# Kernel optimization log

Measured on AMD Instinct MI355X. Metric: run time of the kernel, lower is better.

Reference implementation:

```python
import jax, jax.numpy as jnp
import numpy as np

B, I, O, T, L = 16, 512, 512, 256, 4096
EPS = 1e-8


def setup_inputs() -> dict:
    key = jax.random.key(0)
    ks = jax.random.split(key, 10)
    def lin_w(k, out_d, in_d):  # kaiming-uniform-ish init like torch Linear
        bound = 1.0 / np.sqrt(in_d)
        return jax.random.uniform(k, (out_d, in_d), jnp.float32, -bound, bound)
    return {
        "x": jax.random.normal(ks[0], (B, I, L), jnp.float32),
        "t": jax.random.normal(ks[1], (B, T), jnp.float32),
        "weight": lin_w(ks[2], O, I),            # base conv weight [O, I]
        "W1": lin_w(ks[3], T, T), "b1": jnp.zeros((T,), jnp.float32),
        "W2": lin_w(ks[4], T, T), "b2": jnp.zeros((T,), jnp.float32),
        "W3": lin_w(ks[5], I, T), "b3": jnp.zeros((I,), jnp.float32),
    }


def reference(x, t, weight, W1, b1, W2, b2, W3, b3):
    # mod MLP: Linear -> SiLU -> Linear -> SiLU -> Linear
    h = jax.nn.silu(t @ W1.T + b1)
    h = jax.nn.silu(h @ W2.T + b2)
    s = h @ W3.T + b3 + 1.0                    # [B, I] modulation scales
    bw = weight[None, :, :] * s[:, None, :]    # [B, O, I]
    demod = jax.lax.rsqrt(jnp.sum(bw * bw, axis=2) + EPS)  # [B, O]
    bw = bw * demod[:, :, None]                # demodulated per-sample weights
    # grouped 1x1 conv (groups=B) == batched pointwise contraction
    return jnp.einsum('boi,bil->bol', bw, x)   # [B, O, L]
```

## Files before the change

kernel.cpp:

```cpp
#include <hip/hip_runtime.h>
#include <hip/hip_bf16.h>

typedef float f4v __attribute__((ext_vector_type(4)));
typedef float f32x4 __attribute__((ext_vector_type(4)));
typedef __bf16 bf16x8 __attribute__((ext_vector_type(8)));

#define GLDS16(gsrc, ldst)                                                  \
  __builtin_amdgcn_global_load_lds(                                         \
      (const __attribute__((address_space(1))) unsigned int*)(gsrc),        \
      (__attribute__((address_space(3))) unsigned int*)(ldst), 16, 0, 0)

__device__ __forceinline__ unsigned pack2bf(float lo, float hi) {
  unsigned short ua = __builtin_bit_cast(unsigned short, (__bf16)lo);
  unsigned short ub = __builtin_bit_cast(unsigned short, (__bf16)hi);
  return (unsigned)ua | ((unsigned)ub << 16);
}

__global__ __launch_bounds__(256) void mlp_kernel(
    const float* __restrict__ t,
    const float* __restrict__ W1, const float* __restrict__ b1,
    const float* __restrict__ W2, const float* __restrict__ b2,
    const float* __restrict__ W3, const float* __restrict__ b3,
    float* __restrict__ s_out) {
  __shared__ float tt[256];
  __shared__ float hh[256];
  const int b = blockIdx.x;
  const int tid = threadIdx.x;
  tt[tid] = t[b * 256 + tid];
  __syncthreads();
  float acc = b1[tid];
  {
    const f4v* wrow = (const f4v*)(W1 + tid * 256);
    #pragma unroll 16
    for (int k = 0; k < 64; ++k) {
      f4v wv = wrow[k];
      acc += wv[0] * tt[4 * k] + wv[1] * tt[4 * k + 1] +
             wv[2] * tt[4 * k + 2] + wv[3] * tt[4 * k + 3];
    }
  }
  float h = acc / (1.0f + expf(-acc));
  __syncthreads();
  hh[tid] = h;
  __syncthreads();
  acc = b2[tid];
  {
    const f4v* wrow = (const f4v*)(W2 + tid * 256);
    #pragma unroll 16
    for (int k = 0; k < 64; ++k) {
      f4v wv = wrow[k];
      acc += wv[0] * hh[4 * k] + wv[1] * hh[4 * k + 1] +
             wv[2] * hh[4 * k + 2] + wv[3] * hh[4 * k + 3];
    }
  }
  h = acc / (1.0f + expf(-acc));
  __syncthreads();
  tt[tid] = h;
  __syncthreads();
  #pragma unroll
  for (int rep = 0; rep < 2; ++rep) {
    const int o = rep * 256 + tid;
    float a3 = b3[o];
    const f4v* wrow = (const f4v*)(W3 + o * 256);
    #pragma unroll 16
    for (int k = 0; k < 64; ++k) {
      f4v wv = wrow[k];
      a3 += wv[0] * tt[4 * k] + wv[1] * tt[4 * k + 1] +
            wv[2] * tt[4 * k + 2] + wv[3] * tt[4 * k + 3];
    }
    s_out[b * 512 + o] = a3 + 1.0f;
  }
}

__global__ __launch_bounds__(256) void modw_kernel(
    const float* __restrict__ weight, const float* __restrict__ s_in,
    unsigned short* __restrict__ bwq) {
  const int tid = threadIdx.x;
  const int wid = (blockIdx.x << 2) | (tid >> 6);
  const int b = wid >> 9;
  const int o = wid & 511;
  const int lane = tid & 63;
  const f4v* wp = (const f4v*)(weight + o * 512 + lane * 8);
  const f4v* sp = (const f4v*)(s_in + b * 512 + lane * 8);
  f4v w0 = wp[0], w1 = wp[1];
  f4v s0 = sp[0], s1 = sp[1];
  float p[8];
  p[0] = w0[0] * s0[0]; p[1] = w0[1] * s0[1];
  p[2] = w0[2] * s0[2]; p[3] = w0[3] * s0[3];
  p[4] = w1[0] * s1[0]; p[5] = w1[1] * s1[1];
  p[6] = w1[2] * s1[2]; p[7] = w1[3] * s1[3];
  float ss = 0.0f;
  #pragma unroll
  for (int i = 0; i < 8; ++i) ss += p[i] * p[i];
  #pragma unroll
  for (int off = 32; off; off >>= 1) ss += __shfl_xor(ss, off);
  const float d = rsqrtf(ss + 1e-8f);
  uint4 outw;
  outw.x = pack2bf(p[0] * d, p[1] * d);
  outw.y = pack2bf(p[2] * d, p[3] * d);
  outw.z = pack2bf(p[4] * d, p[5] * d);
  outw.w = pack2bf(p[6] * d, p[7] * d);
  *(uint4*)(bwq + ((size_t)(b * 512 + o)) * 512 + lane * 8) = outw;
}

__global__ __launch_bounds__(256, 2) void gemm_kernel(
    const float* __restrict__ x, const unsigned short* __restrict__ bwq,
    float* __restrict__ out) {
  __shared__ __align__(16) unsigned short As[2][128 * 32];
  __shared__ __align__(16) unsigned short Bs[128 * 32];

  const int bid = blockIdx.x;
  const int swz = ((bid & 7) << 8) | (bid >> 3);
  const int mt = swz & 3;
  const int nt = (swz >> 2) & 31;
  const int bb = swz >> 7;

  const int tid = threadIdx.x;
  const int lane = tid & 63;
  const int wv = tid >> 6;
  const int wr = wv >> 1, wc = wv & 1;

  const unsigned short* abase = bwq + ((size_t)(bb * 512 + mt * 128)) * 512;
  const float* xbase = x + ((size_t)bb * 512) * 4096 + nt * 128;

  const int pq = tid >> 5;
  const int lc = tid & 31;
  const float* xp = xbase + (size_t)(pq * 4) * 4096 + lc * 4;
  const int sw_w = (lc & 3) << 4;
  char* BsB = (char*)Bs;

  const int g0 = tid, g1 = 256 + tid;
  const unsigned short* asrc0 = abase + (g0 >> 2) * 512 + (g0 & 3) * 8;
  const unsigned short* asrc1 = abase + (g1 >> 2) * 512 + (g1 & 3) * 8;

  const int arow = wr * 64 + (lane & 15);
  const int kgo = (lane >> 4) * 8;
  const int nrow0 = wc * 64 + (lane & 15);
  const int sb = (nrow0 >> 2) & 3;
  const int bByte = nrow0 * 64 + (((lane >> 4) ^ sb) << 4);

  f32x4 acc[4][4] = {};

  GLDS16(asrc0, &As[0][g0 * 8]);
  GLDS16(asrc1, &As[0][g1 * 8]);
  f4v v0 = *(const f4v*)(xp);
  f4v v1 = *(const f4v*)(xp + 4096);
  f4v v2 = *(const f4v*)(xp + 8192);
  f4v v3 = *(const f4v*)(xp + 12288);
  f4v t0, t1, t2, t3;

  for (int it = 0; it < 16; ++it) {
    const int cur = it & 1;
    {
      float r0[4] = {v0[0], v0[1], v0[2], v0[3]};
      float r1[4] = {v1[0], v1[1], v1[2], v1[3]};
      float r2[4] = {v2[0], v2[1], v2[2], v2[3]};
      float r3[4] = {v3[0], v3[1], v3[2], v3[3]};
      #pragma unroll
      for (int j = 0; j < 4; ++j) {
        uint2 val;
        val.x = pack2bf(r0[j], r1[j]);
        val.y = pack2bf(r2[j], r3[j]);
        const int n = (lc << 2) + j;
        *(uint2*)(BsB + n * 64 + ((pq * 8) ^ sw_w)) = val;
      }
    }
    __syncthreads();

    if (it < 15) {
      const int k0n = (it + 1) << 5;
      const unsigned short* an0 = asrc0 + k0n;
      const unsigned short* an1 = asrc1 + k0n;
      GLDS16(an0, &As[cur ^ 1][g0 * 8]);
      GLDS16(an1, &As[cur ^ 1][g1 * 8]);
      const float* xn = xp + (size_t)k0n * 4096;
      t0 = *(const f4v*)(xn);
      t1 = *(const f4v*)(xn + 4096);
      t2 = *(const f4v*)(xn + 8192);
      t3 = *(const f4v*)(xn + 12288);
    }

    {
      const unsigned short* ab = &As[cur][0];
      bf16x8 a0 = *(const bf16x8*)(ab + arow * 32 + kgo);
      bf16x8 a1 = *(const bf16x8*)(ab + arow * 32 + 512 + kgo);
      bf16x8 a2 = *(const bf16x8*)(ab + arow * 32 + 1024 + kgo);
      bf16x8 a3 = *(const bf16x8*)(ab + arow * 32 + 1536 + kgo);
      bf16x8 bf0 = *(const bf16x8*)(BsB + bByte);
      bf16x8 bf1 = *(const bf16x8*)(BsB + bByte + 1024);
      bf16x8 bf2 = *(const bf16x8*)(BsB + bByte + 2048);
      bf16x8 bf3 = *(const bf16x8*)(BsB + bByte + 3072);
      acc[0][0] = __builtin_amdgcn_mfma_f32_16x16x32_bf16(a0, bf0, acc[0][0], 0, 0, 0);
      acc[0][1] = __builtin_amdgcn_mfma_f32_16x16x32_bf16(a0, bf1, acc[0][1], 0, 0, 0);
      acc[0][2] = __builtin_amdgcn_mfma_f32_16x16x32_bf16(a0, bf2, acc[0][2], 0, 0, 0);
      acc[0][3] = __builtin_amdgcn_mfma_f32_16x16x32_bf16(a0, bf3, acc[0][3], 0, 0, 0);
      acc[1][0] = __builtin_amdgcn_mfma_f32_16x16x32_bf16(a1, bf0, acc[1][0], 0, 0, 0);
      acc[1][1] = __builtin_amdgcn_mfma_f32_16x16x32_bf16(a1, bf1, acc[1][1], 0, 0, 0);
      acc[1][2] = __builtin_amdgcn_mfma_f32_16x16x32_bf16(a1, bf2, acc[1][2], 0, 0, 0);
      acc[1][3] = __builtin_amdgcn_mfma_f32_16x16x32_bf16(a1, bf3, acc[1][3], 0, 0, 0);
      acc[2][0] = __builtin_amdgcn_mfma_f32_16x16x32_bf16(a2, bf0, acc[2][0], 0, 0, 0);
      acc[2][1] = __builtin_amdgcn_mfma_f32_16x16x32_bf16(a2, bf1, acc[2][1], 0, 0, 0);
      acc[2][2] = __builtin_amdgcn_mfma_f32_16x16x32_bf16(a2, bf2, acc[2][2], 0, 0, 0);
      acc[2][3] = __builtin_amdgcn_mfma_f32_16x16x32_bf16(a2, bf3, acc[2][3], 0, 0, 0);
      acc[3][0] = __builtin_amdgcn_mfma_f32_16x16x32_bf16(a3, bf0, acc[3][0], 0, 0, 0);
      acc[3][1] = __builtin_amdgcn_mfma_f32_16x16x32_bf16(a3, bf1, acc[3][1], 0, 0, 0);
      acc[3][2] = __builtin_amdgcn_mfma_f32_16x16x32_bf16(a3, bf2, acc[3][2], 0, 0, 0);
      acc[3][3] = __builtin_amdgcn_mfma_f32_16x16x32_bf16(a3, bf3, acc[3][3], 0, 0, 0);
    }
    __syncthreads();

    if (it < 15) { v0 = t0; v1 = t1; v2 = t2; v3 = t3; }
  }

  const size_t ob =
      ((size_t)(bb * 512 + mt * 128 + wr * 64 + ((lane >> 4) << 2))) * 4096 +
      nt * 128 + wc * 64 + (lane & 15);
  #pragma unroll
  for (int mi = 0; mi < 4; ++mi)
    #pragma unroll
    for (int ni = 0; ni < 4; ++ni)
      #pragma unroll
      for (int jj = 0; jj < 4; ++jj)
        out[ob + (size_t)(mi * 16 + jj) * 4096 + ni * 16] = acc[mi][ni][jj];
}

extern "C" void kernel_launch(void* const* d_in, const int* in_sizes, int n_in,
                              void* d_out, int out_size, void* d_ws, size_t ws_size,
                              hipStream_t stream) {
  const float* x      = (const float*)d_in[0];
  const float* t      = (const float*)d_in[1];
  const float* weight = (const float*)d_in[2];
  const float* W1     = (const float*)d_in[3];
  const float* b1     = (const float*)d_in[4];
  const float* W2     = (const float*)d_in[5];
  const float* b2     = (const float*)d_in[6];
  const float* W3     = (const float*)d_in[7];
  const float* b3     = (const float*)d_in[8];
  float* out = (float*)d_out;

  float* s_ws = (float*)d_ws;
  unsigned short* bwq = (unsigned short*)((char*)d_ws + 32 * 1024);

  mlp_kernel<<<16, 256, 0, stream>>>(t, W1, b1, W2, b2, W3, b3, s_ws);
  modw_kernel<<<2048, 256, 0, stream>>>(weight, s_ws, bwq);
  gemm_kernel<<<2048, 256, 0, stream>>>(x, bwq, out);
}
```

Measured before the change: 126.2 us.

## Deepen GEMM pipeline to triple-buffered A, double-buffered B with one barrier

Restructures the batched GEMM main loop into a deeper software pipeline. A tiles are triple-buffered via async global-to-LDS loads, B (x converted to bf16) is double-buffered, and x register prefetch runs three steps ahead. The loop is fully unrolled with hand-placed vmcnt waits so each iteration needs one barrier instead of two. This aims to hide global load latency and cut synchronization stalls. It also raises the launch-bounds occupancy hint to 3, at the cost of more registers and LDS per block and fragile manual waitcnt accounting.

```diff
diff --git a/kernel.cpp b/kernel.cpp
--- a/kernel.cpp
+++ b/kernel.cpp
@@ -102,11 +102,11 @@
   *(uint4*)(bwq + ((size_t)(b * 512 + o)) * 512 + lane * 8) = outw;
 }
 
-__global__ __launch_bounds__(256, 2) void gemm_kernel(
+__global__ __launch_bounds__(256, 3) void gemm_kernel(
     const float* __restrict__ x, const unsigned short* __restrict__ bwq,
     float* __restrict__ out) {
-  __shared__ __align__(16) unsigned short As[2][128 * 32];
-  __shared__ __align__(16) unsigned short Bs[128 * 32];
+  __shared__ __align__(16) unsigned short As[3][128 * 32];
+  __shared__ __align__(16) unsigned short Bs[2][128 * 32];
 
   const int bid = blockIdx.x;
   const int swz = ((bid & 7) << 8) | (bid >> 3);
@@ -139,76 +139,99 @@
   const int bByte = nrow0 * 64 + (((lane >> 4) ^ sb) << 4);
 
   f32x4 acc[4][4] = {};
-
-  GLDS16(asrc0, &As[0][g0 * 8]);
-  GLDS16(asrc1, &As[0][g1 * 8]);
-  f4v v0 = *(const f4v*)(xp);
-  f4v v1 = *(const f4v*)(xp + 4096);
-  f4v v2 = *(const f4v*)(xp + 8192);
-  f4v v3 = *(const f4v*)(xp + 12288);
-  f4v t0, t1, t2, t3;
-
+  f4v xv[3][4];
+
+#define LOADX(SET, STEP)                                                    \
+  do {                                                                      \
+    const float* _p = xp + (size_t)((STEP) * 32) * 4096;                    \
+    xv[SET][0] = *(const f4v*)(_p);                                         \
+    xv[SET][1] = *(const f4v*)(_p + 4096);                                  \
+    xv[SET][2] = *(const f4v*)(_p + 8192);                                  \
+    xv[SET][3] = *(const f4v*)(_p + 12288);                                 \
+  } while (0)
+
+#define STAGEA(STEP, BUF)                                                   \
+  do {                                                                      \
+    GLDS16(asrc0 + (STEP) * 32, &As[BUF][g0 * 8]);                          \
+    GLDS16(asrc1 + (STEP) * 32, &As[BUF][g1 * 8]);                          \
+  } while (0)
+
+#define PACKB(SET, BUF)                                                     \
+  do {                                                                      \
+    char* _bs = BsB + (BUF) * 8192;                                         \
+    _Pragma("unroll")                                                       \
+    for (int j = 0; j < 4; ++j) {                                           \
+      uint2 val;                                                            \
+      val.x = pack2bf(xv[SET][0][j], xv[SET][1][j]);                        \
+      val.y = pack2bf(xv[SET][2][j], xv[SET][3][j]);                        \
+      const int n = (lc << 2) + j;                                          \
+      *(uint2*)(_bs + n * 64 + ((pq * 8) ^ sw_w)) = val;                    \
+    }                                                                       \
+  } while (0)
+
+#define FENCE() asm volatile("" ::: "memory")
+#define BARN(N)                                                             \
+  do {                                                                      \
+    asm volatile("s_waitcnt lgkmcnt(0)\n\ts_waitcnt vmcnt(" #N ")" :::      \
+                     "memory");                                             \
+    __builtin_amdgcn_s_barrier();                                           \
+    asm volatile("" ::: "memory");                                          \
+  } while (0)
+
+#define COMPUTE(CA, CB)                                                     \
+  do {                                                                      \
+    const unsigned short* ab = &As[CA][0];                                  \
+    const char* bbuf = BsB + (CB) * 8192;                                   \
+    bf16x8 a0 = *(const bf16x8*)(ab + arow * 32 + kgo);                     \
+    bf16x8 a1 = *(const bf16x8*)(ab + arow * 32 + 512 + kgo);               \
+    bf16x8 a2 = *(const bf16x8*)(ab + arow * 32 + 1024 + kgo);              \
+    bf16x8 a3 = *(const bf16x8*)(ab + arow * 32 + 1536 + kgo);              \
+    bf16x8 bf0 = *(const bf16x8*)(bbuf + bByte);                            \
+    bf16x8 bf1 = *(const bf16x8*)(bbuf + bByte + 1024);                     \
+    bf16x8 bf2 = *(const bf16x8*)(bbuf + bByte + 2048);                     \
+    bf16x8 bf3 = *(const bf16x8*)(bbuf + bByte + 3072);                     \
+    acc[0][0] = __builtin_amdgcn_mfma_f32_16x16x32_bf16(a0, bf0, acc[0][0], 0, 0, 0); \
+    acc[0][1] = __builtin_amdgcn_mfma_f32_16x16x32_bf16(a0, bf1, acc[0][1], 0, 0, 0); \
+    acc[0][2] = __builtin_amdgcn_mfma_f32_16x16x32_bf16(a0, bf2, acc[0][2], 0, 0, 0); \
+    acc[0][3] = __builtin_amdgcn_mfma_f32_16x16x32_bf16(a0, bf3, acc[0][3], 0, 0, 0); \
+    acc[1][0] = __builtin_amdgcn_mfma_f32_16x16x32_bf16(a1, bf0, acc[1][0], 0, 0, 0); \
+    acc[1][1] = __builtin_amdgcn_mfma_f32_16x16x32_bf16(a1, bf1, acc[1][1], 0, 0, 0); \
+    acc[1][2] = __builtin_amdgcn_mfma_f32_16x16x32_bf16(a1, bf2, acc[1][2], 0, 0, 0); \
+    acc[1][3] = __builtin_amdgcn_mfma_f32_16x16x32_bf16(a1, bf3, acc[1][3], 0, 0, 0); \
+    acc[2][0] = __builtin_amdgcn_mfma_f32_16x16x32_bf16(a2, bf0, acc[2][0], 0, 0, 0); \
+    acc[2][1] = __builtin_amdgcn_mfma_f32_16x16x32_bf16(a2, bf1, acc[2][1], 0, 0, 0); \
+    acc[2][2] = __builtin_amdgcn_mfma_f32_16x16x32_bf16(a2, bf2, acc[2][2], 0, 0, 0); \
+    acc[2][3] = __builtin_amdgcn_mfma_f32_16x16x32_bf16(a2, bf3, acc[2][3], 0, 0, 0); \
+    acc[3][0] = __builtin_amdgcn_mfma_f32_16x16x32_bf16(a3, bf0, acc[3][0], 0, 0, 0); \
+    acc[3][1] = __builtin_amdgcn_mfma_f32_16x16x32_bf16(a3, bf1, acc[3][1], 0, 0, 0); \
+    acc[3][2] = __builtin_amdgcn_mfma_f32_16x16x32_bf16(a3, bf2, acc[3][2], 0, 0, 0); \
+    acc[3][3] = __builtin_amdgcn_mfma_f32_16x16x32_bf16(a3, bf3, acc[3][3], 0, 0, 0); \
+  } while (0)
+
+  STAGEA(0, 0);
+  FENCE();
+  LOADX(0, 0);
+  STAGEA(1, 1);
+  FENCE();
+  LOADX(1, 1);
+  LOADX(2, 2);
+  PACKB(0, 0);
+  BARN(10);
+
+  #pragma unroll
   for (int it = 0; it < 16; ++it) {
-    const int cur = it & 1;
-    {
-      float r0[4] = {v0[0], v0[1], v0[2], v0[3]};
-      float r1[4] = {v1[0], v1[1], v1[2], v1[3]};
-      float r2[4] = {v2[0], v2[1], v2[2], v2[3]};
-      float r3[4] = {v3[0], v3[1], v3[2], v3[3]};
-      #pragma unroll
-      for (int j = 0; j < 4; ++j) {
-        uint2 val;
-        val.x = pack2bf(r0[j], r1[j]);
-        val.y = pack2bf(r2[j], r3[j]);
-        const int n = (lc << 2) + j;
-        *(uint2*)(BsB + n * 64 + ((pq * 8) ^ sw_w)) = val;
-      }
-    }
-    __syncthreads();
-
-    if (it < 15) {
-      const int k0n = (it + 1) << 5;
-      const unsigned short* an0 = asrc0 + k0n;
-      const unsigned short* an1 = asrc1 + k0n;
-      GLDS16(an0, &As[cur ^ 1][g0 * 8]);
-      GLDS16(an1, &As[cur ^ 1][g1 * 8]);
-      const float* xn = xp + (size_t)k0n * 4096;
-      t0 = *(const f4v*)(xn);
-      t1 = *(const f4v*)(xn + 4096);
-      t2 = *(const f4v*)(xn + 8192);
-      t3 = *(const f4v*)(xn + 12288);
-    }
-
-    {
-      const unsigned short* ab = &As[cur][0];
-      bf16x8 a0 = *(const bf16x8*)(ab + arow * 32 + kgo);
-      bf16x8 a1 = *(const bf16x8*)(ab + arow * 32 + 512 + kgo);
-      bf16x8 a2 = *(const bf16x8*)(ab + arow * 32 + 1024 + kgo);
-      bf16x8 a3 = *(const bf16x8*)(ab + arow * 32 + 1536 + kgo);
-      bf16x8 bf0 = *(const bf16x8*)(BsB + bByte);
-      bf16x8 bf1 = *(const bf16x8*)(BsB + bByte + 1024);
-      bf16x8 bf2 = *(const bf16x8*)(BsB + bByte + 2048);
-      bf16x8 bf3 = *(const bf16x8*)(BsB + bByte + 3072);
-      acc[0][0] = __builtin_amdgcn_mfma_f32_16x16x32_bf16(a0, bf0, acc[0][0], 0, 0, 0);
-      acc[0][1] = __builtin_amdgcn_mfma_f32_16x16x32_bf16(a0, bf1, acc[0][1], 0, 0, 0);
-      acc[0][2] = __builtin_amdgcn_mfma_f32_16x16x32_bf16(a0, bf2, acc[0][2], 0, 0, 0);
-      acc[0][3] = __builtin_amdgcn_mfma_f32_16x16x32_bf16(a0, bf3, acc[0][3], 0, 0, 0);
-      acc[1][0] = __builtin_amdgcn_mfma_f32_16x16x32_bf16(a1, bf0, acc[1][0], 0, 0, 0);
-      acc[1][1] = __builtin_amdgcn_mfma_f32_16x16x32_bf16(a1, bf1, acc[1][1], 0, 0, 0);
-      acc[1][2] = __builtin_amdgcn_mfma_f32_16x16x32_bf16(a1, bf2, acc[1][2], 0, 0, 0);
-      acc[1][3] = __builtin_amdgcn_mfma_f32_16x16x32_bf16(a1, bf3, acc[1][3], 0, 0, 0);
-      acc[2][0] = __builtin_amdgcn_mfma_f32_16x16x32_bf16(a2, bf0, acc[2][0], 0, 0, 0);
-      acc[2][1] = __builtin_amdgcn_mfma_f32_16x16x32_bf16(a2, bf1, acc[2][1], 0, 0, 0);
-      acc[2][2] = __builtin_amdgcn_mfma_f32_16x16x32_bf16(a2, bf2, acc[2][2], 0, 0, 0);
-      acc[2][3] = __builtin_amdgcn_mfma_f32_16x16x32_bf16(a2, bf3, acc[2][3], 0, 0, 0);
-      acc[3][0] = __builtin_amdgcn_mfma_f32_16x16x32_bf16(a3, bf0, acc[3][0], 0, 0, 0);
-      acc[3][1] = __builtin_amdgcn_mfma_f32_16x16x32_bf16(a3, bf1, acc[3][1], 0, 0, 0);
-      acc[3][2] = __builtin_amdgcn_mfma_f32_16x16x32_bf16(a3, bf2, acc[3][2], 0, 0, 0);
-      acc[3][3] = __builtin_amdgcn_mfma_f32_16x16x32_bf16(a3, bf3, acc[3][3], 0, 0, 0);
-    }
-    __syncthreads();
-
-    if (it < 15) { v0 = t0; v1 = t1; v2 = t2; v3 = t3; }
+    if (it <= 14) PACKB((it + 1) % 3, (it + 1) & 1);
+    if (it <= 13) STAGEA(it + 2, (it + 2) % 3);
+    FENCE();
+    if (it <= 12) LOADX(it % 3, it + 3);
+    COMPUTE(it % 3, it & 1);
+    if (it <= 12) {
+      BARN(10);
+    } else if (it == 13) {
+      BARN(6);
+    } else if (it == 14) {
+      BARN(0);
+    }
   }
 
   const size_t ob =
@@ -221,6 +244,13 @@
       #pragma unroll
       for (int jj = 0; jj < 4; ++jj)
         out[ob + (size_t)(mi * 16 + jj) * 4096 + ni * 16] = acc[mi][ni][jj];
+
+#undef LOADX
+#undef STAGEA
+#undef PACKB
+#undef FENCE
+#undef BARN
+#undef COMPUTE
 }
 
 extern "C" void kernel_launch(void* const* d_in, const int* in_sizes, int n_in,
```

After: 126.4 us. About the same (+0.2%).

## Pre-transpose and cast x to bf16 in a separate kernel, stream both GEMM operands via LDS DMA

Applied to the files above, without the earlier changes.

Adds a kernel that casts x to bf16 and transposes it to [B, L, I] through an XOR-swizzled LDS tile. The GEMM then loads both A and B tiles with global_load_lds directly into swizzled LDS, with no in-loop register conversion. The GEMM also drops double buffering and the occupancy hint, so loads and MFMA are no longer overlapped within a block. The cost is an extra full pass over x: a 128MB fp32 read plus a 64MB bf16 write and later read.

```diff
diff --git a/kernel.cpp b/kernel.cpp
--- a/kernel.cpp
+++ b/kernel.cpp
@@ -102,11 +102,52 @@
   *(uint4*)(bwq + ((size_t)(b * 512 + o)) * 512 + lane * 8) = outw;
 }
 
-__global__ __launch_bounds__(256, 2) void gemm_kernel(
-    const float* __restrict__ x, const unsigned short* __restrict__ bwq,
-    float* __restrict__ out) {
-  __shared__ __align__(16) unsigned short As[2][128 * 32];
-  __shared__ __align__(16) unsigned short Bs[128 * 32];
+__global__ __launch_bounds__(256) void xcastT_kernel(
+    const float* __restrict__ x, unsigned short* __restrict__ xT) {
+  __shared__ unsigned short lds[64 * 128];
+  const int bidx = blockIdx.x;
+  const int lt = bidx & 63;
+  const int it = (bidx >> 6) & 3;
+  const int b  = bidx >> 8;
+  const int tid = threadIdx.x;
+
+  const int l_lo = tid & 15;
+  const int i_pt = tid >> 4;
+  const float* src =
+      x + ((size_t)(b * 512 + it * 128 + i_pt)) * 4096 + lt * 64 + l_lo * 4;
+  #pragma unroll
+  for (int j = 0; j < 8; ++j) {
+    f4v v = *(const f4v*)(src + (size_t)j * 16 * 4096);
+    const int i = j * 16 + i_pt;
+    const int g = i >> 3;
+    #pragma unroll
+    for (int c = 0; c < 4; ++c) {
+      const int l = l_lo * 4 + c;
+      const int pg = g ^ (l & 15);
+      lds[l * 128 + pg * 8 + (i & 7)] =
+          __builtin_bit_cast(unsigned short, (__bf16)v[c]);
+    }
+  }
+  __syncthreads();
+
+  const int l_loc = tid >> 2;
+  const int iq = tid & 3;
+  unsigned short* dst =
+      xT + ((size_t)(b * 4096 + lt * 64 + l_loc)) * 512 + it * 128;
+  #pragma unroll
+  for (int j = 0; j < 4; ++j) {
+    const int gi = iq * 4 + j;
+    const int pg = gi ^ (l_loc & 15);
+    uint4 val = *(const uint4*)&lds[l_loc * 128 + pg * 8];
+    *(uint4*)(dst + gi * 8) = val;
+  }
+}
+
+__global__ __launch_bounds__(256) void gemm_kernel(
+    const unsigned short* __restrict__ xT,
+    const unsigned short* __restrict__ bwq, float* __restrict__ out) {
+  __shared__ __align__(16) unsigned short As[4096];
+  __shared__ __align__(16) unsigned short Bs[4096];
 
   const int bid = blockIdx.x;
   const int swz = ((bid & 7) << 8) | (bid >> 3);
@@ -120,75 +161,55 @@
   const int wr = wv >> 1, wc = wv & 1;
 
   const unsigned short* abase = bwq + ((size_t)(bb * 512 + mt * 128)) * 512;
-  const float* xbase = x + ((size_t)bb * 512) * 4096 + nt * 128;
-
-  const int pq = tid >> 5;
-  const int lc = tid & 31;
-  const float* xp = xbase + (size_t)(pq * 4) * 4096 + lc * 4;
-  const int sw_w = (lc & 3) << 4;
-  char* BsB = (char*)Bs;
-
-  const int g0 = tid, g1 = 256 + tid;
-  const unsigned short* asrc0 = abase + (g0 >> 2) * 512 + (g0 & 3) * 8;
-  const unsigned short* asrc1 = abase + (g1 >> 2) * 512 + (g1 & 3) * 8;
-
-  const int arow = wr * 64 + (lane & 15);
-  const int kgo = (lane >> 4) * 8;
-  const int nrow0 = wc * 64 + (lane & 15);
-  const int sb = (nrow0 >> 2) & 3;
-  const int bByte = nrow0 * 64 + (((lane >> 4) ^ sb) << 4);
+  const unsigned short* bbase = xT + ((size_t)(bb * 4096 + nt * 128)) * 512;
+
+  const int s0 = tid, s1 = 256 + tid;
+  const int kq0 = s0 >> 7, p0 = s0 & 127;
+  const int kq1 = s1 >> 7, p1 = s1 & 127;
+  const int i0 = p0 ^ ((p0 >> 3) & 7);
+  const int i1 = p1 ^ ((p1 >> 3) & 7);
+  const unsigned short* asrc0 = abase + i0 * 512 + kq0 * 8;
+  const unsigned short* asrc1 = abase + i1 * 512 + kq1 * 8;
+  const unsigned short* bsrc0 = bbase + i0 * 512 + kq0 * 8;
+  const unsigned short* bsrc1 = bbase + i1 * 512 + kq1 * 8;
+  unsigned short* adst0 = As + s0 * 8;
+  unsigned short* adst1 = As + s1 * 8;
+  unsigned short* bdst0 = Bs + s0 * 8;
+  unsigned short* bdst1 = Bs + s1 * 8;
+
+  const int kqL = lane >> 4;
+  const int rL = lane & 15;
+  int aro[4], bro[4];
+  #pragma unroll
+  for (int i = 0; i < 4; ++i) {
+    const int m = wr * 64 + i * 16 + rL;
+    aro[i] = kqL * 2048 + (m ^ ((m >> 3) & 7)) * 16;
+    const int n = wc * 64 + i * 16 + rL;
+    bro[i] = kqL * 2048 + (n ^ ((n >> 3) & 7)) * 16;
+  }
 
   f32x4 acc[4][4] = {};
 
-  GLDS16(asrc0, &As[0][g0 * 8]);
-  GLDS16(asrc1, &As[0][g1 * 8]);
-  f4v v0 = *(const f4v*)(xp);
-  f4v v1 = *(const f4v*)(xp + 4096);
-  f4v v2 = *(const f4v*)(xp + 8192);
-  f4v v3 = *(const f4v*)(xp + 12288);
-  f4v t0, t1, t2, t3;
-
+  #pragma unroll
   for (int it = 0; it < 16; ++it) {
-    const int cur = it & 1;
+    const int ko = it * 32;
+    GLDS16(asrc0 + ko, adst0);
+    GLDS16(asrc1 + ko, adst1);
+    GLDS16(bsrc0 + ko, bdst0);
+    GLDS16(bsrc1 + ko, bdst1);
+    __syncthreads();
+
     {
-      float r0[4] = {v0[0], v0[1], v0[2], v0[3]};
-      float r1[4] = {v1[0], v1[1], v1[2], v1[3]};
-      float r2[4] = {v2[0], v2[1], v2[2], v2[3]};
-      float r3[4] = {v3[0], v3[1], v3[2], v3[3]};
-      #pragma unroll
-      for (int j = 0; j < 4; ++j) {
-        uint2 val;
-        val.x = pack2bf(r0[j], r1[j]);
-        val.y = pack2bf(r2[j], r3[j]);
-        const int n = (lc << 2) + j;
-        *(uint2*)(BsB + n * 64 + ((pq * 8) ^ sw_w)) = val;
-      }
-    }
-    __syncthreads();
-
-    if (it < 15) {
-      const int k0n = (it + 1) << 5;
-      const unsigned short* an0 = asrc0 + k0n;
-      const unsigned short* an1 = asrc1 + k0n;
-      GLDS16(an0, &As[cur ^ 1][g0 * 8]);
-      GLDS16(an1, &As[cur ^ 1][g1 * 8]);
-      const float* xn = xp + (size_t)k0n * 4096;
-      t0 = *(const f4v*)(xn);
-      t1 = *(const f4v*)(xn + 4096);
-      t2 = *(const f4v*)(xn + 8192);
-      t3 = *(const f4v*)(xn + 12288);
-    }
-
-    {
-      const unsigned short* ab = &As[cur][0];
-      bf16x8 a0 = *(const bf16x8*)(ab + arow * 32 + kgo);
-      bf16x8 a1 = *(const bf16x8*)(ab + arow * 32 + 512 + kgo);
-      bf16x8 a2 = *(const bf16x8*)(ab + arow * 32 + 1024 + kgo);
-      bf16x8 a3 = *(const bf16x8*)(ab + arow * 32 + 1536 + kgo);
-      bf16x8 bf0 = *(const bf16x8*)(BsB + bByte);
-      bf16x8 bf1 = *(const bf16x8*)(BsB + bByte + 1024);
-      bf16x8 bf2 = *(const bf16x8*)(BsB + bByte + 2048);
-      bf16x8 bf3 = *(const bf16x8*)(BsB + bByte + 3072);
+      const char* ab = (const char*)As;
+      const char* bbuf = (const char*)Bs;
+      bf16x8 a0 = *(const bf16x8*)(ab + aro[0]);
+      bf16x8 a1 = *(const bf16x8*)(ab + aro[1]);
+      bf16x8 a2 = *(const bf16x8*)(ab + aro[2]);
+      bf16x8 a3 = *(const bf16x8*)(ab + aro[3]);
+      bf16x8 bf0 = *(const bf16x8*)(bbuf + bro[0]);
+      bf16x8 bf1 = *(const bf16x8*)(bbuf + bro[1]);
+      bf16x8 bf2 = *(const bf16x8*)(bbuf + bro[2]);
+      bf16x8 bf3 = *(const bf16x8*)(bbuf + bro[3]);
       acc[0][0] = __builtin_amdgcn_mfma_f32_16x16x32_bf16(a0, bf0, acc[0][0], 0, 0, 0);
       acc[0][1] = __builtin_amdgcn_mfma_f32_16x16x32_bf16(a0, bf1, acc[0][1], 0, 0, 0);
       acc[0][2] = __builtin_amdgcn_mfma_f32_16x16x32_bf16(a0, bf2, acc[0][2], 0, 0, 0);
@@ -207,8 +228,6 @@
       acc[3][3] = __builtin_amdgcn_mfma_f32_16x16x32_bf16(a3, bf3, acc[3][3], 0, 0, 0);
     }
     __syncthreads();
-
-    if (it < 15) { v0 = t0; v1 = t1; v2 = t2; v3 = t3; }
   }
 
   const size_t ob =
@@ -239,8 +258,10 @@
 
   float* s_ws = (float*)d_ws;
   unsigned short* bwq = (unsigned short*)((char*)d_ws + 32 * 1024);
+  unsigned short* xTb = (unsigned short*)((char*)d_ws + 32 * 1024 + 8 * 1024 * 1024);
 
   mlp_kernel<<<16, 256, 0, stream>>>(t, W1, b1, W2, b2, W3, b3, s_ws);
+  xcastT_kernel<<<4096, 256, 0, stream>>>(x, xTb);
   modw_kernel<<<2048, 256, 0, stream>>>(weight, s_ws, bwq);
-  gemm_kernel<<<2048, 256, 0, stream>>>(x, bwq, out);
-}
+  gemm_kernel<<<2048, 256, 0, stream>>>(xTb, bwq, out);
+}
```

Result: slower. 161.4 us (+27.9%).
